# Kernel optimization log

Hardware: AMD Instinct MI355X
Metric: run time of the kernel (lower is better)

The kernel has to match this reference:

```python
import jax, jax.numpy as jnp
import numpy as np

NUM_ROUTES = 32 * 6 * 6  # 1152
NUM_CAPS = 10
IN_DIM = 8
OUT_DIM = 16
NUM_ITERS = 3

def _conv(x, w, stride):
    return jax.lax.conv_general_dilated(
        x, w, window_strides=(stride, stride), padding='VALID',
        dimension_numbers=('NCHW', 'OIHW', 'NCHW'))

def _squash(u):
    # squash over last axis, exactly as torch code (no eps)
    sn = (u ** 2).sum(-1, keepdims=True)
    return sn * u / ((1.0 + sn) * jnp.sqrt(sn))

def setup_inputs() -> dict:
    key = jax.random.key(0)
    ks = jax.random.split(key, 10)
    B = 512
    data = jax.random.normal(ks[0], (B, 1, 28, 28), dtype=jnp.float32)
    conv_w = jax.random.normal(ks[1], (256, 1, 9, 9), dtype=jnp.float32) * 0.05
    conv_b = jnp.zeros((256,), dtype=jnp.float32)
    # 8 primary-capsule convs stacked caps-major -> fused conv [8*32,256,9,9]
    pc_w = jax.random.normal(ks[2], (8 * 32, 256, 9, 9), dtype=jnp.float32) * 0.01
    pc_b = jnp.zeros((8 * 32,), dtype=jnp.float32)
    W = jax.random.normal(ks[3], (NUM_ROUTES, NUM_CAPS, OUT_DIM, IN_DIM), dtype=jnp.float32)
    enc_w1 = jax.random.normal(ks[4], (512, OUT_DIM * NUM_CAPS), dtype=jnp.float32) * 0.05
    enc_b1 = jnp.zeros((512,), dtype=jnp.float32)
    enc_w2 = jax.random.normal(ks[5], (9, 512), dtype=jnp.float32) * 0.05
    enc_b2 = jnp.zeros((9,), dtype=jnp.float32)
    return dict(data=data, conv_w=conv_w, conv_b=conv_b, pc_w=pc_w, pc_b=pc_b,
                W=W, enc_w1=enc_w1, enc_b1=enc_b1, enc_w2=enc_w2, enc_b2=enc_b2)

def reference(data, conv_w, conv_b, pc_w, pc_b, W, enc_w1, enc_b1, enc_w2, enc_b2):
    B = data.shape[0]
    # ConvLayer: conv + relu -> [B,256,20,20]
    x = jax.nn.relu(_conv(data, conv_w, 1) + conv_b[None, :, None, None])
    # PrimaryCaps: 8 stride-2 convs (fused, caps-major channels) -> [B,256,6,6]
    u = _conv(x, pc_w, 2) + pc_b[None, :, None, None]
    # torch: stack(dim=1) then view(B, num_routes, -1) == reshape caps-major flat
    u = u.reshape(B, NUM_ROUTES, IN_DIM)
    u = _squash(u)  # [B,R,8]
    # WaferCaps: u_hat[b,r,c,o] = sum_i W[r,c,o,i] * u[b,r,i]
    u_hat = jnp.einsum('rcoi,bri->brco', W, u)  # [B,R,C,O]
    b_ij = jnp.zeros((NUM_ROUTES, NUM_CAPS), dtype=u_hat.dtype)
    v = None
    for it in range(NUM_ITERS):
        c_ij = jax.nn.softmax(b_ij, axis=0)  # softmax over routes (dim=1 in torch)
        s = jnp.einsum('rc,brco->bco', c_ij, u_hat)  # [B,C,O]
        # original squashes [B,1,C,O,1] over last (size-1) dim -> elementwise
        s2 = s ** 2
        v = s2 * s / ((1.0 + s2) * jnp.sqrt(s2))  # = s*|s|/(1+s^2)
        if it < NUM_ITERS - 1:
            a = jnp.einsum('brco,bco->brc', u_hat, v)  # [B,R,C]
            b_ij = b_ij + a.mean(axis=0)
    # Encoder: flatten [B,C,O] row-major -> [B,160]
    flat = v.reshape(B, NUM_CAPS * OUT_DIM)
    h = jax.nn.relu(flat @ enc_w1.T + enc_b1)  # dropout is identity at eval
    out = jax.nn.sigmoid(h @ enc_w2.T + enc_b2)
    return out
```

## Files before the change

kernel.cpp:

```cpp
#include <hip/hip_runtime.h>
#include <hip/hip_bf16.h>
#include <stdint.h>


typedef __bf16 bf16_t;
typedef __bf16 bf16x4 __attribute__((ext_vector_type(4)));
typedef __bf16 bf16x8 __attribute__((ext_vector_type(8)));
typedef float f32x4 __attribute__((ext_vector_type(4)));
typedef int i32x4 __attribute__((ext_vector_type(4)));
typedef int i32x8 __attribute__((ext_vector_type(8)));

__device__ __forceinline__ void gload_lds16(const void* g, void* l) {
    __builtin_amdgcn_global_load_lds((const __attribute__((address_space(1))) void*)g,
                                     (__attribute__((address_space(3))) void*)l, 16, 0, 0);
}

#define MEMBAR() asm volatile("" ::: "memory")

__device__ __forceinline__ uint8_t fp8b(float v) {
    return (uint8_t)(__builtin_amdgcn_cvt_pk_fp8_f32(v, 0.f, 0, false) & 0xFF);
}

__global__ void k_prep(const float* __restrict__ w1, const float* __restrict__ cw,
                       float* __restrict__ w1t, bf16_t* __restrict__ Bc1,
                       float* __restrict__ bij) {
    int blk = blockIdx.x, tid = threadIdx.x;
    if (blk < 45) {
        int i = blk * 256 + tid;
        if (i < 11520) bij[i] = 0.f;
    } else if (blk < 365) {
        int i = (blk - 45) * 256 + tid;
        int j = i / 160, k = i % 160;
        w1t[k * 512 + j] = w1[i];
    } else {
        int i = (blk - 365) * 256 + tid;
        if (i < 26624) {
            int oc = i / 104, k = i % 104;
            Bc1[i] = (k < 81) ? (bf16_t)cw[oc * 81 + k] : (bf16_t)0.f;
        }
    }
}

__global__ __launch_bounds__(256) void k_w2t(const float* __restrict__ pcw,
                                             uint8_t* __restrict__ w2t8) {
    __shared__ uint16_t tmp16[10368];
    int oc = blockIdx.x, tid = threadIdx.x;
    const float* src = pcw + (size_t)oc * 20736;
    for (int q2 = tid; q2 < 10368; q2 += 256) {
        float a = src[q2 * 2] * 64.f;
        float b = src[q2 * 2 + 1] * 64.f;
        uint32_t pk = __builtin_amdgcn_cvt_pk_fp8_f32(a, b, 0, false);
        tmp16[q2] = (uint16_t)(pk & 0xFFFF);
    }
    __syncthreads();
    uint32_t* dst = (uint32_t*)(w2t8 + (size_t)oc * 20736);
    for (int w = tid; w < 5184; w += 256) {
        int k = w * 4;
        int t = k >> 8, ic0 = k & 255;
        uint32_t r = 0;
#pragma unroll
        for (int j = 0; j < 4; ++j) {
            int s = (ic0 + j) * 81 + t;
            uint32_t b = (tmp16[s >> 1] >> ((s & 1) * 8)) & 0xFF;
            r |= b << (8 * j);
        }
        dst[w] = r;
    }
}

__global__ __launch_bounds__(512) void k_c1gemm(const float* __restrict__ data,
                                                const bf16_t* __restrict__ Bc1,
                                                const float* __restrict__ cb,
                                                uint8_t* __restrict__ xt8) {
    __shared__ __align__(16) bf16_t As[128 * 104];
    __shared__ __align__(16) bf16_t Bs[256 * 104];
    int tid = threadIdx.x, lane = tid & 63, wave = tid >> 6;
    int wm = wave >> 2, wn = wave & 3;
    for (int i = tid; i < 3328; i += 512) {
        int byte = i * 16;
        int r = byte / 208;
        int c16 = (byte - r * 208) >> 4;
        gload_lds16(Bc1 + r * 104 + c16 * 8, (char*)Bs + byte);
    }
    int mr = wm * 64 + (lane & 15);
    int nr = wn * 64 + (lane & 15);
    float bias[4];
#pragma unroll
    for (int nj = 0; nj < 4; ++nj) bias[nj] = cb[nr + nj * 16];

    for (int t = 0; t < 2; ++t) {
        int m0 = (blockIdx.x + t * 800) * 128;
        __syncthreads();
        for (int e = tid; e < 13312; e += 512) {
            int r = e / 104, k = e - r * 104;
            int m = m0 + r;
            int b = m / 400, pos = m - b * 400;
            int oh = pos / 20, ow = pos - oh * 20;
            float x = 0.f;
            if (k < 81) {
                int kh = k / 9, kw = k - kh * 9;
                x = data[(size_t)b * 784 + (oh + kh) * 28 + ow + kw];
            }
            As[e] = (bf16_t)x;
        }
        asm volatile("s_waitcnt vmcnt(0)" ::: "memory");
        __syncthreads();
        f32x4 acc[4][4];
#pragma unroll
        for (int mi = 0; mi < 4; ++mi)
#pragma unroll
            for (int nj = 0; nj < 4; ++nj) acc[mi][nj] = (f32x4){0.f, 0.f, 0.f, 0.f};
#pragma unroll
        for (int kk = 0; kk < 3; ++kk) {
            int ch = (kk * 4 + (lane >> 4)) * 8;
            bf16x8 af[4], bfr[4];
#pragma unroll
            for (int i = 0; i < 4; ++i) af[i] = *(const bf16x8*)&As[(mr + i * 16) * 104 + ch];
#pragma unroll
            for (int j = 0; j < 4; ++j) bfr[j] = *(const bf16x8*)&Bs[(nr + j * 16) * 104 + ch];
#pragma unroll
            for (int mi = 0; mi < 4; ++mi)
#pragma unroll
                for (int nj = 0; nj < 4; ++nj)
                    acc[mi][nj] = __builtin_amdgcn_mfma_f32_16x16x32_bf16(af[mi], bfr[nj], acc[mi][nj], 0, 0, 0);
        }
        int mbase = m0 + wm * 64 + (lane >> 4) * 4;
#pragma unroll
        for (int mi = 0; mi < 4; ++mi)
#pragma unroll
            for (int nj = 0; nj < 4; ++nj)
#pragma unroll
                for (int j = 0; j < 4; ++j)
                    xt8[(size_t)(mbase + mi * 16 + j) * 256 + nr + nj * 16] =
                        fp8b(fmaxf(acc[mi][nj][j] + bias[nj], 0.f));
    }
}

__global__ __launch_bounds__(256) void k_pcgemm(const uint8_t* __restrict__ xt8,
                                                const uint8_t* __restrict__ w2t8,
                                                bf16_t* __restrict__ parts) {
    __shared__ __align__(16) uint8_t As[128 * 128];
    __shared__ __align__(16) uint8_t Bs[128 * 128];
    int bid = blockIdx.x;
    int mt = bid % 144;
    int nt = (bid / 144) & 1;
    int ks = bid / 288;
    int m0 = mt * 128, n0 = nt * 128;
    int tid = threadIdx.x, lane = tid & 63, wave = tid >> 6;

    int csrc = (tid & 7) ^ ((tid >> 3) & 7);
    int arow[4];
#pragma unroll
    for (int p = 0; p < 4; ++p) {
        int m = m0 + p * 32 + (tid >> 3);
        int bb = m / 36, pos = m % 36;
        int oh = pos / 6, ow = pos % 6;
        arow[p] = ((bb * 20 + oh * 2) * 20 + ow * 2) * 256;
    }
    const uint8_t* bbase = w2t8 + (size_t)(n0 + (tid >> 3)) * 20736 + csrc * 16;

    f32x4 acc[4][4];
#pragma unroll
    for (int mi = 0; mi < 4; ++mi)
#pragma unroll
        for (int ni = 0; ni < 4; ++ni) acc[mi][ni] = (f32x4){0.f, 0.f, 0.f, 0.f};

    int g0 = ks * 81;
    int mr = (wave >> 1) * 64 + (lane & 15);
    int nr = (wave & 1) * 64 + (lane & 15);
    int rx = lane & 7;
    int c0 = (2 * (lane >> 4)) ^ rx;
    int c1 = (2 * (lane >> 4) + 1) ^ rx;

    for (int it = 0; it < 81; ++it) {
        int g = g0 + it;
        int t = g >> 1, icb = g & 1;
        int kh = t / 9, kw = t - (t / 9) * 9;
        int aoff = (kh * 20 + kw) * 256 + icb * 128 + csrc * 16;
#pragma unroll
        for (int p = 0; p < 4; ++p) {
            gload_lds16(xt8 + arow[p] + aoff, &As[p * 4096 + tid * 16]);
            gload_lds16(bbase + (size_t)p * 32 * 20736 + (size_t)g * 128, &Bs[p * 4096 + tid * 16]);
        }
        __syncthreads();
        i32x8 af[4], bfr[4];
#pragma unroll
        for (int i = 0; i < 4; ++i) {
            i32x4 lo = *(const i32x4*)&As[(mr + i * 16) * 128 + c0 * 16];
            i32x4 hi = *(const i32x4*)&As[(mr + i * 16) * 128 + c1 * 16];
            af[i][0] = lo[0]; af[i][1] = lo[1]; af[i][2] = lo[2]; af[i][3] = lo[3];
            af[i][4] = hi[0]; af[i][5] = hi[1]; af[i][6] = hi[2]; af[i][7] = hi[3];
        }
#pragma unroll
        for (int i = 0; i < 4; ++i) {
            i32x4 lo = *(const i32x4*)&Bs[(nr + i * 16) * 128 + c0 * 16];
            i32x4 hi = *(const i32x4*)&Bs[(nr + i * 16) * 128 + c1 * 16];
            bfr[i][0] = lo[0]; bfr[i][1] = lo[1]; bfr[i][2] = lo[2]; bfr[i][3] = lo[3];
            bfr[i][4] = hi[0]; bfr[i][5] = hi[1]; bfr[i][6] = hi[2]; bfr[i][7] = hi[3];
        }
#pragma unroll
        for (int mi = 0; mi < 4; ++mi)
#pragma unroll
            for (int ni = 0; ni < 4; ++ni)
                acc[mi][ni] = __builtin_amdgcn_mfma_scale_f32_16x16x128_f8f6f4(
                    af[mi], bfr[ni], acc[mi][ni], 0, 0, 0, 0x7F7F7F7F, 0, 0x79797979);
        __syncthreads();
    }

    bf16_t* out = parts + (size_t)ks * 4718592;
    int mbase = m0 + (wave >> 1) * 64 + (lane >> 4) * 4;
    int nbase = n0 + (wave & 1) * 64 + (lane & 15);
#pragma unroll
    for (int mi = 0; mi < 4; ++mi)
#pragma unroll
        for (int ni = 0; ni < 4; ++ni)
#pragma unroll
            for (int j = 0; j < 4; ++j)
                out[(size_t)(mbase + mi * 16 + j) * 256 + nbase + ni * 16] = (bf16_t)acc[mi][ni][j];
}

__global__ __launch_bounds__(256) void k_squash(const bf16_t* __restrict__ parts,
                                                const float* __restrict__ pcb,
                                                bf16_t* __restrict__ ub) {
    __shared__ float s[36 * 257];
    int b = blockIdx.x, tid = threadIdx.x;
    for (int i = tid; i < 9216; i += 256) {
        float a = pcb[i & 255];
#pragma unroll
        for (int p = 0; p < 2; ++p) a += (float)parts[(size_t)p * 4718592 + (size_t)b * 9216 + i];
        s[(i >> 8) * 257 + (i & 255)] = a;
    }
    __syncthreads();
    for (int r = tid; r < 1152; r += 256) {
        int flat0 = r * 8;
        float val[8], sn = 0.f;
#pragma unroll
        for (int e = 0; e < 8; ++e) {
            int f = flat0 + e;
            float x = s[(f % 36) * 257 + f / 36];
            val[e] = x;
            sn += x * x;
        }
        float scale = sn / ((1.f + sn) * sqrtf(sn));
        bf16x8 vv;
#pragma unroll
        for (int e = 0; e < 8; ++e) vv[e] = (bf16_t)(val[e] * scale);
        *(bf16x8*)&ub[(size_t)b * 9216 + flat0] = vv;
    }
}

__global__ __launch_bounds__(256) void k_uT(const bf16_t* __restrict__ ub, bf16_t* __restrict__ uT) {
    __shared__ bf16_t t[64 * 66];
    int kt = blockIdx.x % 144, bt = blockIdx.x / 144;
    int k0 = kt * 64, b0 = bt * 64;
    int tid = threadIdx.x;
    int c8 = tid & 7;
#pragma unroll
    for (int p = 0; p < 2; ++p) {
        int r = p * 32 + (tid >> 3);
        bf16x8 vv = *(const bf16x8*)&ub[(size_t)(b0 + r) * 9216 + k0 + c8 * 8];
        uint32_t u4[4];
        *(bf16x8*)u4 = vv;
#pragma unroll
        for (int j2 = 0; j2 < 4; ++j2)
            *(uint32_t*)&t[r * 66 + c8 * 8 + j2 * 2] = u4[j2];
    }
    __syncthreads();
#pragma unroll
    for (int p = 0; p < 2; ++p) {
        int kp = p * 32 + (tid >> 3);
        bf16x8 vv;
#pragma unroll
        for (int j = 0; j < 8; ++j) vv[j] = t[(c8 * 8 + j) * 66 + kp];
        *(bf16x8*)&uT[(size_t)(k0 + kp) * 512 + b0 + c8 * 8] = vv;
    }
}

__global__ void k_cij(const float* __restrict__ bij, float* __restrict__ cij) {
    __shared__ float red[256];
    int c = blockIdx.x, tid = threadIdx.x;
    float mx = -1e30f;
    for (int r = tid; r < 1152; r += 256) mx = fmaxf(mx, bij[r * 10 + c]);
    red[tid] = mx; __syncthreads();
    for (int s = 128; s > 0; s >>= 1) { if (tid < s) red[tid] = fmaxf(red[tid], red[tid + s]); __syncthreads(); }
    float MX = red[0]; __syncthreads();
    float sm = 0.f;
    for (int r = tid; r < 1152; r += 256) sm += expf(bij[r * 10 + c] - MX);
    red[tid] = sm; __syncthreads();
    for (int s = 128; s > 0; s >>= 1) { if (tid < s) red[tid] += red[tid + s]; __syncthreads(); }
    float inv = 1.f / red[0];
    for (int r = tid; r < 1152; r += 256) cij[r * 10 + c] = expf(bij[r * 10 + c] - MX) * inv;
}

__global__ void k_fold(const float* __restrict__ cij, const float* __restrict__ W,
                       bf16_t* __restrict__ cw2T) {
    int idx = blockIdx.x * 256 + threadIdx.x;
    int co = idx / 9216, k = idx % 9216;
    int r = k >> 3, i = k & 7;
    int c = co >> 4, o = co & 15;
    cw2T[idx] = (bf16_t)(cij[r * 10 + c] * W[((size_t)(r * 10 + c) * 16 + o) * 8 + i]);
}

__global__ __launch_bounds__(256) void k_rgemm(const bf16_t* __restrict__ A,
                                               const bf16_t* __restrict__ B,
                                               bf16_t* __restrict__ Cp,
                                               int Kfull, int steps, int mtiles) {
    __shared__ __align__(16) bf16_t As[64 * 64];
    __shared__ __align__(16) bf16_t Bs[160 * 64];
    int bid = blockIdx.x;
    int mt = bid % mtiles, ks = bid / mtiles;
    int m0 = mt * 64;
    int k0 = ks * steps * 64;
    int tid = threadIdx.x, lane = tid & 63, wave = tid >> 6;
    int srow = tid >> 3;
    int csrc = (tid & 7) ^ (srow & 7);
    const bf16_t* asrc[2];
    const bf16_t* bsrc[5];
#pragma unroll
    for (int p = 0; p < 2; ++p)
        asrc[p] = A + (size_t)(m0 + p * 32 + srow) * Kfull + k0 + csrc * 8;
#pragma unroll
    for (int p = 0; p < 5; ++p)
        bsrc[p] = B + (size_t)(p * 32 + srow) * Kfull + k0 + csrc * 8;

    f32x4 acc[2][5];
#pragma unroll
    for (int mi = 0; mi < 2; ++mi)
#pragma unroll
        for (int nj = 0; nj < 5; ++nj) acc[mi][nj] = (f32x4){0.f, 0.f, 0.f, 0.f};

    int mr = (wave >> 1) * 32 + (lane & 15);
    int nr = (wave & 1) * 80 + (lane & 15);
    int rx = lane & 7;

    for (int it = 0; it < steps; ++it) {
#pragma unroll
        for (int p = 0; p < 2; ++p) gload_lds16(asrc[p] + it * 64, As + p * 2048 + tid * 8);
#pragma unroll
        for (int p = 0; p < 5; ++p) gload_lds16(bsrc[p] + it * 64, Bs + p * 2048 + tid * 8);
        __syncthreads();
#pragma unroll
        for (int kk = 0; kk < 2; ++kk) {
            int ch = ((kk * 4 + (lane >> 4)) ^ rx) * 8;
            bf16x8 af[2], bfr[5];
#pragma unroll
            for (int i = 0; i < 2; ++i) af[i] = *(const bf16x8*)&As[(mr + i * 16) * 64 + ch];
#pragma unroll
            for (int j = 0; j < 5; ++j) bfr[j] = *(const bf16x8*)&Bs[(nr + j * 16) * 64 + ch];
#pragma unroll
            for (int mi = 0; mi < 2; ++mi)
#pragma unroll
                for (int nj = 0; nj < 5; ++nj)
                    acc[mi][nj] = __builtin_amdgcn_mfma_f32_16x16x32_bf16(af[mi], bfr[nj], acc[mi][nj], 0, 0, 0);
        }
        __syncthreads();
    }

    bf16_t* out = Cp + (size_t)ks * ((size_t)mtiles * 64 * 160);
    int mbase = m0 + (wave >> 1) * 32 + (lane >> 4) * 4;
    int nbase = (wave & 1) * 80 + (lane & 15);
#pragma unroll
    for (int mi = 0; mi < 2; ++mi)
#pragma unroll
        for (int nj = 0; nj < 5; ++nj)
#pragma unroll
            for (int j = 0; j < 4; ++j)
                out[(size_t)(mbase + mi * 16 + j) * 160 + nbase + nj * 16] = (bf16_t)acc[mi][nj][j];
}

__global__ void k_vcomp(const bf16_t* __restrict__ sp, float* __restrict__ v,
                        bf16_t* __restrict__ vT) {
    int idx = blockIdx.x * 256 + threadIdx.x;
    float s = 0.f;
#pragma unroll
    for (int p = 0; p < 36; ++p) s += (float)sp[(size_t)p * 81920 + idx];
    float val = s * fabsf(s) / (1.f + s * s);
    v[idx] = val;
    int b = idx / 160, co = idx % 160;
    vT[(size_t)co * 512 + b] = (bf16_t)val;
}

__global__ __launch_bounds__(256) void k_ggemm2(const bf16_t* __restrict__ uT,
                                                const bf16_t* __restrict__ vT,
                                                const float* __restrict__ W,
                                                float* __restrict__ bij) {
    __shared__ __align__(16) bf16_t As[64 * 64];
    __shared__ __align__(16) bf16_t Bs[160 * 64];
    __shared__ float Gl[64 * 161];
    int mt = blockIdx.x;
    int m0 = mt * 64;
    int tid = threadIdx.x, lane = tid & 63, wave = tid >> 6;
    int srow = tid >> 3;
    int csrc = (tid & 7) ^ (srow & 7);
    const bf16_t* asrc[2];
    const bf16_t* bsrc[5];
#pragma unroll
    for (int p = 0; p < 2; ++p)
        asrc[p] = uT + (size_t)(m0 + p * 32 + srow) * 512 + csrc * 8;
#pragma unroll
    for (int p = 0; p < 5; ++p)
        bsrc[p] = vT + (size_t)(p * 32 + srow) * 512 + csrc * 8;

    f32x4 acc[2][5];
#pragma unroll
    for (int mi = 0; mi < 2; ++mi)
#pragma unroll
        for (int nj = 0; nj < 5; ++nj) acc[mi][nj] = (f32x4){0.f, 0.f, 0.f, 0.f};

    int mr = (wave >> 1) * 32 + (lane & 15);
    int nr = (wave & 1) * 80 + (lane & 15);
    int rx = lane & 7;

    for (int it = 0; it < 8; ++it) {
#pragma unroll
        for (int p = 0; p < 2; ++p) gload_lds16(asrc[p] + it * 64, As + p * 2048 + tid * 8);
#pragma unroll
        for (int p = 0; p < 5; ++p) gload_lds16(bsrc[p] + it * 64, Bs + p * 2048 + tid * 8);
        __syncthreads();
#pragma unroll
        for (int kk = 0; kk < 2; ++kk) {
            int ch = ((kk * 4 + (lane >> 4)) ^ rx) * 8;
            bf16x8 af[2], bfr[5];
#pragma unroll
            for (int i = 0; i < 2; ++i) af[i] = *(const bf16x8*)&As[(mr + i * 16) * 64 + ch];
#pragma unroll
            for (int j = 0; j < 5; ++j) bfr[j] = *(const bf16x8*)&Bs[(nr + j * 16) * 64 + ch];
#pragma unroll
            for (int mi = 0; mi < 2; ++mi)
#pragma unroll
                for (int nj = 0; nj < 5; ++nj)
                    acc[mi][nj] = __builtin_amdgcn_mfma_f32_16x16x32_bf16(af[mi], bfr[nj], acc[mi][nj], 0, 0, 0);
        }
        __syncthreads();
    }

    int mbl = (wave >> 1) * 32 + (lane >> 4) * 4;
    int nbase = (wave & 1) * 80 + (lane & 15);
#pragma unroll
    for (int mi = 0; mi < 2; ++mi)
#pragma unroll
        for (int nj = 0; nj < 5; ++nj)
#pragma unroll
            for (int j = 0; j < 4; ++j)
                Gl[(mbl + mi * 16 + j) * 161 + nbase + nj * 16] = acc[mi][nj][j] * (1.0f / 512.0f);
    __syncthreads();
    if (tid < 80) {
        int rl = tid / 10, c = tid % 10;
        int r = mt * 8 + rl;
        const float* wbase = W + (size_t)(r * 10 + c) * 128;
        float s = 0.f;
#pragma unroll
        for (int o = 0; o < 16; ++o)
#pragma unroll
            for (int i = 0; i < 8; ++i)
                s += wbase[o * 8 + i] * Gl[(rl * 8 + i) * 161 + c * 16 + o];
        bij[r * 10 + c] += s;
    }
}

__global__ __launch_bounds__(256) void k_enc(const float* __restrict__ v,
                                             const float* __restrict__ w1t,
                                             const float* __restrict__ b1,
                                             const float* __restrict__ w2,
                                             const float* __restrict__ b2,
                                             float* __restrict__ out) {
    __shared__ float fl[160];
    __shared__ float h[512];
    int b = blockIdx.x, tid = threadIdx.x;
    if (tid < 160) fl[tid] = v[b * 160 + tid];
    __syncthreads();
    for (int j = tid; j < 512; j += 256) {
        float s = b1[j];
#pragma unroll 8
        for (int k = 0; k < 160; ++k) s += fl[k] * w1t[k * 512 + j];
        h[j] = fmaxf(s, 0.f);
    }
    __syncthreads();
    int wave = tid >> 6, lane = tid & 63;
    for (int j = wave; j < 9; j += 4) {
        float p = 0.f;
#pragma unroll
        for (int l = lane; l < 512; l += 64) p += h[l] * w2[j * 512 + l];
#pragma unroll
        for (int off = 32; off > 0; off >>= 1) p += __shfl_down(p, off, 64);
        if (lane == 0) out[b * 9 + j] = 1.f / (1.f + expf(-(p + b2[j])));
    }
}

extern "C" void kernel_launch(void* const* d_in, const int* in_sizes, int n_in,
                              void* d_out, int out_size, void* d_ws, size_t ws_size,
                              hipStream_t stream) {
    const float* data   = (const float*)d_in[0];
    const float* conv_w = (const float*)d_in[1];
    const float* conv_b = (const float*)d_in[2];
    const float* pc_w   = (const float*)d_in[3];
    const float* pc_b   = (const float*)d_in[4];
    const float* W      = (const float*)d_in[5];
    const float* enc_w1 = (const float*)d_in[6];
    const float* enc_b1 = (const float*)d_in[7];
    const float* enc_w2 = (const float*)d_in[8];
    const float* enc_b2 = (const float*)d_in[9];

    char* ws = (char*)d_ws;
    uint8_t* xt8   = (uint8_t*)(ws + 0);
    uint8_t* w2t8  = (uint8_t*)(ws + 52428800);
    bf16_t*  parts = (bf16_t*)(ws + 57737216);
    bf16_t*  uT    = (bf16_t*)(ws + 76611584);
    bf16_t*  cw2T  = (bf16_t*)(ws + 86048768);
    bf16_t*  sp    = (bf16_t*)(ws + 88997888);
    bf16_t*  ub    = (bf16_t*)(ws + 94896128);
    float*   v     = (float*)(ws + 104333312);
    bf16_t*  vT    = (bf16_t*)(ws + 104660992);
    float*   w1t   = (float*)(ws + 104824832);
    float*   bij   = (float*)(ws + 105152512);
    float*   cij   = (float*)(ws + 105198592);
    bf16_t*  Bc1   = (bf16_t*)(ws + 105244672);
    float*   outp  = (float*)d_out;

    hipLaunchKernelGGL(k_prep, dim3(469), dim3(256), 0, stream, enc_w1, conv_w, w1t, Bc1, bij);
    hipLaunchKernelGGL(k_w2t, dim3(256), dim3(256), 0, stream, pc_w, w2t8);
    hipLaunchKernelGGL(k_c1gemm, dim3(800), dim3(512), 0, stream, data, Bc1, conv_b, xt8);
    hipLaunchKernelGGL(k_pcgemm, dim3(576), dim3(256), 0, stream, xt8, w2t8, parts);
    hipLaunchKernelGGL(k_squash, dim3(512), dim3(256), 0, stream, parts, pc_b, ub);
    hipLaunchKernelGGL(k_uT, dim3(1152), dim3(256), 0, stream, ub, uT);
    for (int it = 0; it < 3; ++it) {
        hipLaunchKernelGGL(k_cij, dim3(10), dim3(256), 0, stream, bij, cij);
        hipLaunchKernelGGL(k_fold, dim3(5760), dim3(256), 0, stream, cij, W, cw2T);
        hipLaunchKernelGGL(k_rgemm, dim3(288), dim3(256), 0, stream, ub, cw2T, sp, 9216, 4, 8);
        hipLaunchKernelGGL(k_vcomp, dim3(320), dim3(256), 0, stream, sp, v, vT);
        if (it < 2) {
            hipLaunchKernelGGL(k_ggemm2, dim3(144), dim3(256), 0, stream, uT, vT, W, bij);
        }
    }
    hipLaunchKernelGGL(k_enc, dim3(512), dim3(256), 0, stream, v, w1t, enc_b1, enc_w2, enc_b2, outp);
}
```

Before: 331.5 us.

## Double-buffer pcgemm LDS loads, vectorize conv1 im2col, skip first softmax

The primary-capsule FP8 GEMM now uses two LDS buffers, so the next K-slice's global-to-LDS loads are issued before the current slice's MFMAs run. This is meant to overlap load latency with compute, at the cost of doubling that kernel's shared memory. The conv1 im2col fill now copies 9 contiguous pixels per row and zero-fills only the padding columns, which removes per-element divisions. On the first routing iteration the coefficients are uniform, so a dedicated fold kernel scales W by 1/1152 directly and skips the softmax launch.

```diff
diff --git a/kernel.cpp b/kernel.cpp
--- a/kernel.cpp
+++ b/kernel.cpp
@@ -91,17 +91,19 @@
     for (int t = 0; t < 2; ++t) {
         int m0 = (blockIdx.x + t * 800) * 128;
         __syncthreads();
-        for (int e = tid; e < 13312; e += 512) {
-            int r = e / 104, k = e - r * 104;
+        for (int z = tid; z < 128 * 23; z += 512) {
+            int r = z / 23, k = 81 + z - (z / 23) * 23;
+            As[r * 104 + k] = (bf16_t)0.f;
+        }
+        for (int pr = tid; pr < 1152; pr += 512) {
+            int r = pr / 9, kh = pr - (pr / 9) * 9;
             int m = m0 + r;
             int b = m / 400, pos = m - b * 400;
             int oh = pos / 20, ow = pos - oh * 20;
-            float x = 0.f;
-            if (k < 81) {
-                int kh = k / 9, kw = k - kh * 9;
-                x = data[(size_t)b * 784 + (oh + kh) * 28 + ow + kw];
-            }
-            As[e] = (bf16_t)x;
+            const float* src = data + (size_t)b * 784 + (oh + kh) * 28 + ow;
+            bf16_t* dst = &As[r * 104 + kh * 9];
+#pragma unroll
+            for (int j = 0; j < 9; ++j) dst[j] = (bf16_t)src[j];
         }
         asm volatile("s_waitcnt vmcnt(0)" ::: "memory");
         __syncthreads();
@@ -139,8 +141,8 @@
 __global__ __launch_bounds__(256) void k_pcgemm(const uint8_t* __restrict__ xt8,
                                                 const uint8_t* __restrict__ w2t8,
                                                 bf16_t* __restrict__ parts) {
-    __shared__ __align__(16) uint8_t As[128 * 128];
-    __shared__ __align__(16) uint8_t Bs[128 * 128];
+    __shared__ __align__(16) uint8_t As[2 * 16384];
+    __shared__ __align__(16) uint8_t Bs[2 * 16384];
     int bid = blockIdx.x;
     int mt = bid % 144;
     int nt = (bid / 144) & 1;
@@ -172,29 +174,38 @@
     int c0 = (2 * (lane >> 4)) ^ rx;
     int c1 = (2 * (lane >> 4) + 1) ^ rx;
 
+#define PCSTAGE(BUF, G) do {                                                       \
+        int g_ = (G);                                                              \
+        int t_ = g_ >> 1, icb_ = g_ & 1;                                           \
+        int kh_ = t_ / 9, kw_ = t_ - (t_ / 9) * 9;                                 \
+        int aoff_ = (kh_ * 20 + kw_) * 256 + icb_ * 128 + csrc * 16;               \
+        _Pragma("unroll")                                                          \
+        for (int p = 0; p < 4; ++p) {                                              \
+            gload_lds16(xt8 + arow[p] + aoff_, &As[(BUF) * 16384 + p * 4096 + tid * 16]); \
+            gload_lds16(bbase + (size_t)p * 32 * 20736 + (size_t)g_ * 128,         \
+                        &Bs[(BUF) * 16384 + p * 4096 + tid * 16]);                 \
+        }                                                                          \
+    } while (0)
+
+    PCSTAGE(0, g0);
+    asm volatile("s_waitcnt vmcnt(0)" ::: "memory");
+    MEMBAR(); __builtin_amdgcn_s_barrier(); MEMBAR();
+
     for (int it = 0; it < 81; ++it) {
-        int g = g0 + it;
-        int t = g >> 1, icb = g & 1;
-        int kh = t / 9, kw = t - (t / 9) * 9;
-        int aoff = (kh * 20 + kw) * 256 + icb * 128 + csrc * 16;
-#pragma unroll
-        for (int p = 0; p < 4; ++p) {
-            gload_lds16(xt8 + arow[p] + aoff, &As[p * 4096 + tid * 16]);
-            gload_lds16(bbase + (size_t)p * 32 * 20736 + (size_t)g * 128, &Bs[p * 4096 + tid * 16]);
-        }
-        __syncthreads();
+        int cur = (it & 1) * 16384;
+        if (it < 80) PCSTAGE((it + 1) & 1, g0 + it + 1);
         i32x8 af[4], bfr[4];
 #pragma unroll
         for (int i = 0; i < 4; ++i) {
-            i32x4 lo = *(const i32x4*)&As[(mr + i * 16) * 128 + c0 * 16];
-            i32x4 hi = *(const i32x4*)&As[(mr + i * 16) * 128 + c1 * 16];
+            i32x4 lo = *(const i32x4*)&As[cur + (mr + i * 16) * 128 + c0 * 16];
+            i32x4 hi = *(const i32x4*)&As[cur + (mr + i * 16) * 128 + c1 * 16];
             af[i][0] = lo[0]; af[i][1] = lo[1]; af[i][2] = lo[2]; af[i][3] = lo[3];
             af[i][4] = hi[0]; af[i][5] = hi[1]; af[i][6] = hi[2]; af[i][7] = hi[3];
         }
 #pragma unroll
         for (int i = 0; i < 4; ++i) {
-            i32x4 lo = *(const i32x4*)&Bs[(nr + i * 16) * 128 + c0 * 16];
-            i32x4 hi = *(const i32x4*)&Bs[(nr + i * 16) * 128 + c1 * 16];
+            i32x4 lo = *(const i32x4*)&Bs[cur + (nr + i * 16) * 128 + c0 * 16];
+            i32x4 hi = *(const i32x4*)&Bs[cur + (nr + i * 16) * 128 + c1 * 16];
             bfr[i][0] = lo[0]; bfr[i][1] = lo[1]; bfr[i][2] = lo[2]; bfr[i][3] = lo[3];
             bfr[i][4] = hi[0]; bfr[i][5] = hi[1]; bfr[i][6] = hi[2]; bfr[i][7] = hi[3];
         }
@@ -204,8 +215,10 @@
             for (int ni = 0; ni < 4; ++ni)
                 acc[mi][ni] = __builtin_amdgcn_mfma_scale_f32_16x16x128_f8f6f4(
                     af[mi], bfr[ni], acc[mi][ni], 0, 0, 0, 0x7F7F7F7F, 0, 0x79797979);
-        __syncthreads();
-    }
+        asm volatile("s_waitcnt vmcnt(0)" ::: "memory");
+        MEMBAR(); __builtin_amdgcn_s_barrier(); MEMBAR();
+    }
+#undef PCSTAGE
 
     bf16_t* out = parts + (size_t)ks * 4718592;
     int mbase = m0 + (wave >> 1) * 64 + (lane >> 4) * 4;
@@ -299,6 +312,14 @@
     int r = k >> 3, i = k & 7;
     int c = co >> 4, o = co & 15;
     cw2T[idx] = (bf16_t)(cij[r * 10 + c] * W[((size_t)(r * 10 + c) * 16 + o) * 8 + i]);
+}
+
+__global__ void k_fold0(const float* __restrict__ W, bf16_t* __restrict__ cw2T) {
+    int idx = blockIdx.x * 256 + threadIdx.x;
+    int co = idx / 9216, k = idx % 9216;
+    int r = k >> 3, i = k & 7;
+    int c = co >> 4, o = co & 15;
+    cw2T[idx] = (bf16_t)(W[((size_t)(r * 10 + c) * 16 + o) * 8 + i] * (1.0f / 1152.0f));
 }
 
 __global__ __launch_bounds__(256) void k_rgemm(const bf16_t* __restrict__ A,
@@ -524,8 +545,12 @@
     hipLaunchKernelGGL(k_squash, dim3(512), dim3(256), 0, stream, parts, pc_b, ub);
     hipLaunchKernelGGL(k_uT, dim3(1152), dim3(256), 0, stream, ub, uT);
     for (int it = 0; it < 3; ++it) {
-        hipLaunchKernelGGL(k_cij, dim3(10), dim3(256), 0, stream, bij, cij);
-        hipLaunchKernelGGL(k_fold, dim3(5760), dim3(256), 0, stream, cij, W, cw2T);
+        if (it == 0) {
+            hipLaunchKernelGGL(k_fold0, dim3(5760), dim3(256), 0, stream, W, cw2T);
+        } else {
+            hipLaunchKernelGGL(k_cij, dim3(10), dim3(256), 0, stream, bij, cij);
+            hipLaunchKernelGGL(k_fold, dim3(5760), dim3(256), 0, stream, cij, W, cw2T);
+        }
         hipLaunchKernelGGL(k_rgemm, dim3(288), dim3(256), 0, stream, ub, cw2T, sp, 9216, 4, 8);
         hipLaunchKernelGGL(k_vcomp, dim3(320), dim3(256), 0, stream, sp, v, vT);
         if (it < 2) {
```

New measurement: 340.3 us. +2.7%, slower.
